# Kernel tuning notes

Measured on AMD Instinct MI355X. Metric: run time of the kernel, lower is better.

The kernel has to match this reference:

```python
import jax, jax.numpy as jnp
import numpy as np

D_MODEL = 768
NUM_HEADS = 12
HEAD_DIM = D_MODEL // NUM_HEADS
B, T = 2, 4096


def setup_inputs() -> dict:
    key = jax.random.key(0)
    k1, k2, k3, k4, k5 = jax.random.split(key, 5)
    s_in = 1.0 / np.sqrt(D_MODEL)
    return {
        "x": jax.random.normal(k1, (B, T, D_MODEL), dtype=jnp.float32),
        "w_qkv": jax.random.normal(k2, (3 * D_MODEL, D_MODEL), dtype=jnp.float32) * s_in,
        "b_qkv": jax.random.normal(k3, (3 * D_MODEL,), dtype=jnp.float32) * 0.01,
        "w_out": jax.random.normal(k4, (D_MODEL, D_MODEL), dtype=jnp.float32) * s_in,
        "b_out": jax.random.normal(k5, (D_MODEL,), dtype=jnp.float32) * 0.01,
    }


def reference(x, w_qkv, b_qkv, w_out, b_out):
    b, t, c = x.shape
    # qkv: [B,T,3C] -> [3,B,H,T,Dh]  (torch Linear: x @ W.T + b)
    qkv = (x @ w_qkv.T + b_qkv).reshape(b, t, 3, NUM_HEADS, HEAD_DIM)
    qkv = jnp.transpose(qkv, (2, 0, 3, 1, 4))
    q, k, v = qkv[0], qkv[1], qkv[2]
    scale = 1.0 / np.sqrt(HEAD_DIM)
    scores = jnp.einsum("bhqd,bhkd->bhqk", q, k) * scale  # [B,H,T,T]
    causal = jnp.tril(jnp.ones((t, t), dtype=bool))
    scores = jnp.where(causal, scores, -jnp.inf)
    weights = jax.nn.softmax(scores, axis=-1)
    out = jnp.einsum("bhqk,bhkd->bhqd", weights, v)  # [B,H,T,Dh]
    out = jnp.transpose(out, (0, 2, 1, 3)).reshape(b, t, c)
    return out @ w_out.T + b_out
```

## Files before the change

kernel.cpp:

```cpp
#include <hip/hip_runtime.h>


#define NHEADS 12
#define DHEAD  64
#define TSEQ   4096
#define BATCH  2
#define CMODEL 768
#define MTOT   (BATCH * TSEQ)
#define NQKV   (3 * CMODEL)

typedef __attribute__((ext_vector_type(8))) short s16x8;
typedef __attribute__((ext_vector_type(4))) float f32x4;
typedef __attribute__((ext_vector_type(4))) unsigned short u16x4;
typedef __attribute__((ext_vector_type(2))) unsigned int u32x2;

__device__ __forceinline__ unsigned short f2bf(float f) {
    unsigned u = __builtin_bit_cast(unsigned, f);
    u += 0x7fffu + ((u >> 16) & 1u);
    return (unsigned short)(u >> 16);
}

__device__ __forceinline__ unsigned pk2bf(float a, float b) {
    return (unsigned)f2bf(a) | ((unsigned)f2bf(b) << 16);
}

__device__ __forceinline__ unsigned pkpos(float a, float b) {
    unsigned ua = __builtin_bit_cast(unsigned, a) + 0x8000u;
    unsigned ub = __builtin_bit_cast(unsigned, b) + 0x8000u;
    return (ua >> 16) | (ub & 0xffff0000u);
}

__device__ __forceinline__ float fexp2(float x) {
    return __builtin_amdgcn_exp2f(x);
}

__device__ __forceinline__ void async_load16(const void* g, void* l) {
    __builtin_amdgcn_global_load_lds(
        (const __attribute__((address_space(1))) unsigned*)g,
        (__attribute__((address_space(3))) unsigned*)l, 16, 0, 0);
}

__global__ __launch_bounds__(256) void cvt3_kernel(
    const float* __restrict__ s0, const float* __restrict__ s1,
    const float* __restrict__ s2,
    unsigned short* __restrict__ d0, unsigned short* __restrict__ d1,
    unsigned short* __restrict__ d2, int n0, int n1, int n2)
{
    int i = blockIdx.x * 256 + threadIdx.x;
    const float* s; unsigned short* d; int j;
    if (i < n0)                { s = s0; d = d0; j = i; }
    else if (i < n0 + n1)      { s = s1; d = d1; j = i - n0; }
    else if (i < n0 + n1 + n2) { s = s2; d = d2; j = i - n0 - n1; }
    else return;
    f32x4 v = ((const f32x4*)s)[j];
    u32x2 o;
    o.x = pk2bf(v.x, v.y);
    o.y = pk2bf(v.z, v.w);
    ((u32x2*)d)[j] = o;
}

__global__ __launch_bounds__(256) void gemm_qkv_kernel(
    const unsigned short* __restrict__ A,
    const unsigned short* __restrict__ Bw,
    const float* __restrict__ bias,
    unsigned short* __restrict__ Qb,
    unsigned short* __restrict__ Kb,
    unsigned short* __restrict__ Vt)
{
    __shared__ unsigned short sA[128][64];
    __shared__ unsigned short sB[128][64];
    const int n0 = blockIdx.x * 128;
    const int m0 = blockIdx.y * 128;
    const int tid = threadIdx.x;
    const int l = tid & 63, g = l >> 4, l15 = l & 15;
    const int w = tid >> 6, wm = w & 1, wn = w >> 1;
    const int wbase = tid & 192;
    const int seg = n0 / 768;

    f32x4 acc[4][4];
#pragma unroll
    for (int a = 0; a < 4; a++)
#pragma unroll
        for (int b = 0; b < 4; b++) acc[a][b] = (f32x4){0.f, 0.f, 0.f, 0.f};

    if (seg < 2) {
        for (int k0 = 0; k0 < 768; k0 += 64) {
#pragma unroll
            for (int i = 0; i < 4; i++) {
                const int idx = i * 256 + tid;
                const int row = idx >> 3, pc = idx & 7;
                const int lc = pc ^ (row & 7);
                async_load16(&A[(size_t)(m0 + row) * 768 + k0 + lc * 8],
                             &sA[0][0] + (size_t)(i * 256 + wbase) * 8);
                async_load16(&Bw[(size_t)(n0 + row) * 768 + k0 + lc * 8],
                             &sB[0][0] + (size_t)(i * 256 + wbase) * 8);
            }
            __syncthreads();
#pragma unroll
            for (int ks = 0; ks < 2; ks++) {
                const int cc = ((ks * 4 + g) ^ (l15 & 7)) * 8;
                s16x8 af[4], bf[4];
#pragma unroll
                for (int mt = 0; mt < 4; mt++)
                    af[mt] = *(const s16x8*)&sA[wm * 64 + mt * 16 + l15][cc];
#pragma unroll
                for (int nt = 0; nt < 4; nt++)
                    bf[nt] = *(const s16x8*)&sB[wn * 64 + nt * 16 + l15][cc];
#pragma unroll
                for (int nt = 0; nt < 4; nt++)
#pragma unroll
                    for (int mt = 0; mt < 4; mt++)
                        acc[nt][mt] = __builtin_amdgcn_mfma_f32_16x16x32_bf16(
                            bf[nt], af[mt], acc[nt][mt], 0, 0, 0);
            }
            __syncthreads();
        }

        unsigned short* dst = (seg == 0) ? Qb : Kb;
        const float sc = (seg == 0) ? 0.18033688011f : 1.0f;
        const int hh = ((n0 - seg * 768) + wn * 64) >> 6;
#pragma unroll
        for (int nt = 0; nt < 4; nt++) {
            const int dh = nt * 16 + g * 4;
            const f32x4 bv4 = *(const f32x4*)&bias[n0 + wn * 64 + dh];
#pragma unroll
            for (int mt = 0; mt < 4; mt++) {
                const int m = m0 + wm * 64 + mt * 16 + l15;
                const int b = m >> 12, t = m & 4095;
                u32x2 pk;
                pk.x = pk2bf((acc[nt][mt][0] + bv4[0]) * sc,
                             (acc[nt][mt][1] + bv4[1]) * sc);
                pk.y = pk2bf((acc[nt][mt][2] + bv4[2]) * sc,
                             (acc[nt][mt][3] + bv4[3]) * sc);
                *(u32x2*)&dst[(((size_t)(b * NHEADS + hh) * TSEQ + t) << 6) + dh] = pk;
            }
        }
    } else {
        for (int k0 = 0; k0 < 768; k0 += 64) {
#pragma unroll
            for (int i = 0; i < 4; i++) {
                const int idx = i * 256 + tid;
                const int row = idx >> 3, pc = idx & 7;
                const int lc = pc ^ (row & 7);
                async_load16(&A[(size_t)(m0 + row) * 768 + k0 + lc * 8],
                             &sA[0][0] + (size_t)(i * 256 + wbase) * 8);
                async_load16(&Bw[(size_t)(n0 + row) * 768 + k0 + lc * 8],
                             &sB[0][0] + (size_t)(i * 256 + wbase) * 8);
            }
            __syncthreads();
#pragma unroll
            for (int ks = 0; ks < 2; ks++) {
                const int cc = ((ks * 4 + g) ^ (l15 & 7)) * 8;
                s16x8 af[4], bf[4];
#pragma unroll
                for (int mt = 0; mt < 4; mt++)
                    af[mt] = *(const s16x8*)&sA[wm * 64 + mt * 16 + l15][cc];
#pragma unroll
                for (int nt = 0; nt < 4; nt++)
                    bf[nt] = *(const s16x8*)&sB[wn * 64 + nt * 16 + l15][cc];
#pragma unroll
                for (int mt = 0; mt < 4; mt++)
#pragma unroll
                    for (int nt = 0; nt < 4; nt++)
                        acc[mt][nt] = __builtin_amdgcn_mfma_f32_16x16x32_bf16(
                            af[mt], bf[nt], acc[mt][nt], 0, 0, 0);
            }
            __syncthreads();
        }

#pragma unroll
        for (int nt = 0; nt < 4; nt++) {
            const int n = n0 + wn * 64 + nt * 16 + l15;
            const float bv = bias[n];
            const int hh = (n - 1536) >> 6;
            const int dh = n & 63;
#pragma unroll
            for (int mt = 0; mt < 4; mt++) {
                const int mg = m0 + wm * 64 + mt * 16 + g * 4;
                const int b = mg >> 12, t = mg & 4095;
                u32x2 pk;
                pk.x = pk2bf(acc[mt][nt][0] + bv, acc[mt][nt][1] + bv);
                pk.y = pk2bf(acc[mt][nt][2] + bv, acc[mt][nt][3] + bv);
                *(u32x2*)&Vt[((size_t)(b * NHEADS + hh) * DHEAD + dh) * TSEQ + t] = pk;
            }
        }
    }
}


__global__ __launch_bounds__(256, 3) void attn_kernel(
    const unsigned short* __restrict__ Qb,
    const unsigned short* __restrict__ Kb,
    const unsigned short* __restrict__ Vt,
    unsigned short* __restrict__ Ob)
{
    __shared__ unsigned short sK[2][64][64];
    __shared__ unsigned short sV[2][64][64];
    __shared__ unsigned short sPT[4][2][16][64];
    const int bh = blockIdx.x;
    const int jq = 31 - blockIdx.y;
    const int q0 = jq * 128;
    const int ntiles = 2 * jq + 2;
    const int tid = threadIdx.x;
    const int w = tid >> 6, l = tid & 63, g = l >> 4, l15 = l & 15;
    const int wbase = tid & 192;
    const int xk = l15 & 7;

    const int qg0 = q0 + w * 32 + l15;
    const int qg1 = qg0 + 16;

    const unsigned short* Qp0 = Qb + ((size_t)bh * TSEQ + qg0) * DHEAD;
    const unsigned short* Qp1 = Qb + ((size_t)bh * TSEQ + qg1) * DHEAD;
    s16x8 qa[2][2];
    qa[0][0] = *(const s16x8*)&Qp0[g * 8];
    qa[0][1] = *(const s16x8*)&Qp0[32 + g * 8];
    qa[1][0] = *(const s16x8*)&Qp1[g * 8];
    qa[1][1] = *(const s16x8*)&Qp1[32 + g * 8];

    s16x8 vones;
#pragma unroll
    for (int e = 0; e < 8; e++) vones[e] = (short)0x3F80;

    f32x4 o[2][4];
#pragma unroll
    for (int nt = 0; nt < 4; nt++) {
        o[0][nt] = (f32x4){0.f, 0.f, 0.f, 0.f};
        o[1][nt] = (f32x4){0.f, 0.f, 0.f, 0.f};
    }
    f32x4 lac[2];
    lac[0] = (f32x4){0.f, 0.f, 0.f, 0.f};
    lac[1] = (f32x4){0.f, 0.f, 0.f, 0.f};

    const unsigned short* Kbase = Kb + (size_t)bh * TSEQ * DHEAD;
    const unsigned short* Vbase = Vt + (size_t)bh * DHEAD * TSEQ;

    auto stage = [&](int jt, int buf) {
        const int kt = jt * 64;
#pragma unroll
        for (int p = 0; p < 2; p++) {
            const int idx = p * 256 + tid;
            const int row = idx >> 3, pc = idx & 7;
            const int lc = pc ^ (row & 7);
            async_load16(&Kbase[(size_t)(kt + row) * DHEAD + lc * 8],
                         &sK[buf][0][0] + (size_t)(p * 256 + wbase) * 8);
            async_load16(&Vbase[(size_t)row * TSEQ + kt + lc * 8],
                         &sV[buf][0][0] + (size_t)(p * 256 + wbase) * 8);
        }
    };

    stage(0, 0);
    __syncthreads();

    for (int jt = 0; jt < ntiles; jt++) {
        const int buf = jt & 1;
        if (jt + 1 < ntiles) stage(jt + 1, buf ^ 1);
        const int kt = jt * 64;

        f32x4 st[2][4];
#pragma unroll
        for (int nt = 0; nt < 4; nt++) {
            st[0][nt] = (f32x4){0.f, 0.f, 0.f, 0.f};
            st[1][nt] = (f32x4){0.f, 0.f, 0.f, 0.f};
        }
#pragma unroll
        for (int ks = 0; ks < 2; ks++) {
            const int cc = ((ks * 4 + g) ^ xk) * 8;
#pragma unroll
            for (int nt = 0; nt < 4; nt++) {
                const s16x8 akf = *(const s16x8*)&sK[buf][nt * 16 + l15][cc];
                st[0][nt] = __builtin_amdgcn_mfma_f32_16x16x32_bf16(
                    akf, qa[0][ks], st[0][nt], 0, 0, 0);
                st[1][nt] = __builtin_amdgcn_mfma_f32_16x16x32_bf16(
                    akf, qa[1][ks], st[1][nt], 0, 0, 0);
            }
        }

        if (jt >= ntiles - 2) {
#pragma unroll
            for (int nt = 0; nt < 4; nt++)
#pragma unroll
                for (int r = 0; r < 4; r++) {
                    const int key = kt + nt * 16 + g * 4 + r;
                    if (key > qg0) st[0][nt][r] = -1e30f;
                    if (key > qg1) st[1][nt][r] = -1e30f;
                }
        }

#pragma unroll
        for (int qf = 0; qf < 2; qf++) {
#pragma unroll
            for (int nt = 0; nt < 4; nt++) {
                float p0 = fexp2(st[qf][nt][0]);
                float p1 = fexp2(st[qf][nt][1]);
                float p2 = fexp2(st[qf][nt][2]);
                float p3 = fexp2(st[qf][nt][3]);
                u32x2 pk;
                pk.x = pkpos(p0, p1);
                pk.y = pkpos(p2, p3);
                const int phys = ((nt * 2 + (g >> 1)) ^ xk) * 8 + (g & 1) * 4;
                *(u32x2*)&sPT[w][qf][l15][phys] = pk;
            }
        }

#pragma unroll
        for (int ks = 0; ks < 2; ks++) {
            const int cc = ((ks * 4 + g) ^ xk) * 8;
            const s16x8 bp0 = *(const s16x8*)&sPT[w][0][l15][cc];
            const s16x8 bp1 = *(const s16x8*)&sPT[w][1][l15][cc];
#pragma unroll
            for (int nt = 0; nt < 4; nt++) {
                const s16x8 avf = *(const s16x8*)&sV[buf][nt * 16 + l15][cc];
                o[0][nt] = __builtin_amdgcn_mfma_f32_16x16x32_bf16(
                    avf, bp0, o[0][nt], 0, 0, 0);
                o[1][nt] = __builtin_amdgcn_mfma_f32_16x16x32_bf16(
                    avf, bp1, o[1][nt], 0, 0, 0);
            }
            lac[0] = __builtin_amdgcn_mfma_f32_16x16x32_bf16(vones, bp0, lac[0], 0, 0, 0);
            lac[1] = __builtin_amdgcn_mfma_f32_16x16x32_bf16(vones, bp1, lac[1], 0, 0, 0);
        }
        __syncthreads();
    }

    const int b = bh / NHEADS, h = bh - b * NHEADS;
#pragma unroll
    for (int qf = 0; qf < 2; qf++) {
        const int qg = (qf == 0) ? qg0 : qg1;
        const float inv = 1.0f / lac[qf][0];
#pragma unroll
        for (int nt = 0; nt < 4; nt++) {
            u32x2 pk;
            pk.x = pk2bf(o[qf][nt][0] * inv, o[qf][nt][1] * inv);
            pk.y = pk2bf(o[qf][nt][2] * inv, o[qf][nt][3] * inv);
            *(u32x2*)&Ob[((size_t)b * TSEQ + qg) * CMODEL + h * DHEAD + nt * 16 + g * 4] = pk;
        }
    }
}

__global__ __launch_bounds__(256) void gemm_out_kernel(
    const unsigned short* __restrict__ A,
    const unsigned short* __restrict__ Bw,
    const float* __restrict__ bias,
    float* __restrict__ out)
{
    __shared__ unsigned short sA[128][64];
    __shared__ unsigned short sB[128][64];
    const int n0 = blockIdx.x * 128;
    const int m0 = blockIdx.y * 128;
    const int tid = threadIdx.x;
    const int l = tid & 63, g = l >> 4, l15 = l & 15;
    const int w = tid >> 6, wm = w & 1, wn = w >> 1;
    const int wbase = tid & 192;

    f32x4 acc[4][4];
#pragma unroll
    for (int mt = 0; mt < 4; mt++)
#pragma unroll
        for (int nt = 0; nt < 4; nt++) acc[mt][nt] = (f32x4){0.f, 0.f, 0.f, 0.f};

    for (int k0 = 0; k0 < 768; k0 += 64) {
#pragma unroll
        for (int i = 0; i < 4; i++) {
            const int idx = i * 256 + tid;
            const int row = idx >> 3, pc = idx & 7;
            const int lc = pc ^ (row & 7);
            async_load16(&A[(size_t)(m0 + row) * 768 + k0 + lc * 8],
                         &sA[0][0] + (size_t)(i * 256 + wbase) * 8);
            async_load16(&Bw[(size_t)(n0 + row) * 768 + k0 + lc * 8],
                         &sB[0][0] + (size_t)(i * 256 + wbase) * 8);
        }
        __syncthreads();
#pragma unroll
        for (int ks = 0; ks < 2; ks++) {
            const int cc = ((ks * 4 + g) ^ (l15 & 7)) * 8;
            s16x8 af[4], bf[4];
#pragma unroll
            for (int mt = 0; mt < 4; mt++)
                af[mt] = *(const s16x8*)&sA[wm * 64 + mt * 16 + l15][cc];
#pragma unroll
            for (int nt = 0; nt < 4; nt++)
                bf[nt] = *(const s16x8*)&sB[wn * 64 + nt * 16 + l15][cc];
#pragma unroll
            for (int mt = 0; mt < 4; mt++)
#pragma unroll
                for (int nt = 0; nt < 4; nt++)
                    acc[mt][nt] = __builtin_amdgcn_mfma_f32_16x16x32_bf16(
                        af[mt], bf[nt], acc[mt][nt], 0, 0, 0);
        }
        __syncthreads();
    }

#pragma unroll
    for (int nt = 0; nt < 4; nt++) {
        const int n = n0 + wn * 64 + nt * 16 + l15;
        const float bv = bias[n];
#pragma unroll
        for (int mt = 0; mt < 4; mt++)
#pragma unroll
            for (int r = 0; r < 4; r++) {
                const int m = m0 + wm * 64 + mt * 16 + g * 4 + r;
                out[(size_t)m * CMODEL + n] = acc[mt][nt][r] + bv;
            }
    }
}

extern "C" void kernel_launch(void* const* d_in, const int* in_sizes, int n_in,
                              void* d_out, int out_size, void* d_ws, size_t ws_size,
                              hipStream_t stream) {
    const float* x     = (const float*)d_in[0];
    const float* w_qkv = (const float*)d_in[1];
    const float* b_qkv = (const float*)d_in[2];
    const float* w_out = (const float*)d_in[3];
    const float* b_out = (const float*)d_in[4];
    float* out = (float*)d_out;

    char* ws = (char*)d_ws;
    size_t off = 0;
    auto alloc = [&](size_t bytes) -> unsigned short* {
        unsigned short* p = (unsigned short*)(ws + off);
        off += (bytes + 255) & ~(size_t)255;
        return p;
    };
    unsigned short* xb    = alloc((size_t)MTOT * CMODEL * 2);
    unsigned short* wqkvb = alloc((size_t)NQKV * CMODEL * 2);
    unsigned short* woutb = alloc((size_t)CMODEL * CMODEL * 2);
    unsigned short* Qb    = alloc((size_t)BATCH * NHEADS * TSEQ * DHEAD * 2);
    unsigned short* Kb    = alloc((size_t)BATCH * NHEADS * TSEQ * DHEAD * 2);
    unsigned short* Vt    = alloc((size_t)BATCH * NHEADS * TSEQ * DHEAD * 2);
    unsigned short* Ob    = alloc((size_t)MTOT * CMODEL * 2);

    const int n40 = MTOT * CMODEL / 4;
    const int n41 = NQKV * CMODEL / 4;
    const int n42 = CMODEL * CMODEL / 4;
    const int nblk = (n40 + n41 + n42 + 255) / 256;
    cvt3_kernel<<<dim3(nblk), 256, 0, stream>>>(
        x, w_qkv, w_out, xb, wqkvb, woutb, n40, n41, n42);

    gemm_qkv_kernel<<<dim3(NQKV / 128, MTOT / 128), 256, 0, stream>>>(
        xb, wqkvb, b_qkv, Qb, Kb, Vt);
    attn_kernel<<<dim3(BATCH * NHEADS, 32), 256, 0, stream>>>(Qb, Kb, Vt, Ob);
    gemm_out_kernel<<<dim3(CMODEL / 128, MTOT / 128), 256, 0, stream>>>(
        Ob, woutb, b_out, out);
}
```

Measured before the change: 239.6 us.

## Balance causal attention work by pairing query blocks and splitting across two workgroups

Each workgroup now processes a short query block together with its mirrored long one, so every workgroup does 33 key tiles instead of 2 to 64. The long block's key range is split between the two workgroups of a pair. Each writes partial fp32 outputs and row sums to a workspace, and the second to finish combines them, coordinated by an atomic counter. That counter is zeroed in the convert kernel. This removes load imbalance and tail effects from the triangular causal workload, at the cost of extra partial-result traffic, fences, atomics and more live registers.

```diff
diff --git a/kernel.cpp b/kernel.cpp
--- a/kernel.cpp
+++ b/kernel.cpp
@@ -8,6 +8,7 @@
 #define CMODEL 768
 #define MTOT   (BATCH * TSEQ)
 #define NQKV   (3 * CMODEL)
+#define NBH    (BATCH * NHEADS)
 
 typedef __attribute__((ext_vector_type(8))) short s16x8;
 typedef __attribute__((ext_vector_type(4))) float f32x4;
@@ -44,9 +45,11 @@
     const float* __restrict__ s0, const float* __restrict__ s1,
     const float* __restrict__ s2,
     unsigned short* __restrict__ d0, unsigned short* __restrict__ d1,
-    unsigned short* __restrict__ d2, int n0, int n1, int n2)
+    unsigned short* __restrict__ d2, int n0, int n1, int n2,
+    unsigned* __restrict__ flags)
 {
     int i = blockIdx.x * 256 + threadIdx.x;
+    if (i < NBH * 16) flags[i] = 0;
     const float* s; unsigned short* d; int j;
     if (i < n0)                { s = s0; d = d0; j = i; }
     else if (i < n0 + n1)      { s = s1; d = d1; j = i - n0; }
@@ -187,151 +190,236 @@
     }
 }
 
+__device__ __forceinline__ void process_tile(
+    const unsigned short (&sKb)[64][64],
+    const unsigned short (&sVb)[64][64],
+    unsigned short (&sPTw)[2][16][64],
+    const s16x8 (&qa)[2][2],
+    f32x4 (&o)[2][4], f32x4 (&lac)[2],
+    s16x8 vones, int kt, int qg0, bool mask, int g, int l15)
+{
+    const int xk = l15 & 7;
+    const int qg1 = qg0 + 16;
+
+    f32x4 st[2][4];
+#pragma unroll
+    for (int nt = 0; nt < 4; nt++) {
+        st[0][nt] = (f32x4){0.f, 0.f, 0.f, 0.f};
+        st[1][nt] = (f32x4){0.f, 0.f, 0.f, 0.f};
+    }
+#pragma unroll
+    for (int ks = 0; ks < 2; ks++) {
+        const int cc = ((ks * 4 + g) ^ xk) * 8;
+#pragma unroll
+        for (int nt = 0; nt < 4; nt++) {
+            const s16x8 akf = *(const s16x8*)&sKb[nt * 16 + l15][cc];
+            st[0][nt] = __builtin_amdgcn_mfma_f32_16x16x32_bf16(
+                akf, qa[0][ks], st[0][nt], 0, 0, 0);
+            st[1][nt] = __builtin_amdgcn_mfma_f32_16x16x32_bf16(
+                akf, qa[1][ks], st[1][nt], 0, 0, 0);
+        }
+    }
+
+    if (mask) {
+#pragma unroll
+        for (int nt = 0; nt < 4; nt++)
+#pragma unroll
+            for (int r = 0; r < 4; r++) {
+                const int key = kt + nt * 16 + g * 4 + r;
+                if (key > qg0) st[0][nt][r] = -1e30f;
+                if (key > qg1) st[1][nt][r] = -1e30f;
+            }
+    }
+
+#pragma unroll
+    for (int qf = 0; qf < 2; qf++) {
+#pragma unroll
+        for (int nt = 0; nt < 4; nt++) {
+            float p0 = fexp2(st[qf][nt][0]);
+            float p1 = fexp2(st[qf][nt][1]);
+            float p2 = fexp2(st[qf][nt][2]);
+            float p3 = fexp2(st[qf][nt][3]);
+            u32x2 pk;
+            pk.x = pkpos(p0, p1);
+            pk.y = pkpos(p2, p3);
+            const int phys = ((nt * 2 + (g >> 1)) ^ xk) * 8 + (g & 1) * 4;
+            *(u32x2*)&sPTw[qf][l15][phys] = pk;
+        }
+    }
+
+#pragma unroll
+    for (int ks = 0; ks < 2; ks++) {
+        const int cc = ((ks * 4 + g) ^ xk) * 8;
+        const s16x8 bp0 = *(const s16x8*)&sPTw[0][l15][cc];
+        const s16x8 bp1 = *(const s16x8*)&sPTw[1][l15][cc];
+#pragma unroll
+        for (int nt = 0; nt < 4; nt++) {
+            const s16x8 avf = *(const s16x8*)&sVb[nt * 16 + l15][cc];
+            o[0][nt] = __builtin_amdgcn_mfma_f32_16x16x32_bf16(
+                avf, bp0, o[0][nt], 0, 0, 0);
+            o[1][nt] = __builtin_amdgcn_mfma_f32_16x16x32_bf16(
+                avf, bp1, o[1][nt], 0, 0, 0);
+        }
+        lac[0] = __builtin_amdgcn_mfma_f32_16x16x32_bf16(vones, bp0, lac[0], 0, 0, 0);
+        lac[1] = __builtin_amdgcn_mfma_f32_16x16x32_bf16(vones, bp1, lac[1], 0, 0, 0);
+    }
+}
 
 __global__ __launch_bounds__(256, 3) void attn_kernel(
     const unsigned short* __restrict__ Qb,
     const unsigned short* __restrict__ Kb,
     const unsigned short* __restrict__ Vt,
-    unsigned short* __restrict__ Ob)
+    unsigned short* __restrict__ Ob,
+    float* __restrict__ oPart,
+    float* __restrict__ lPart,
+    unsigned* __restrict__ flags)
 {
     __shared__ unsigned short sK[2][64][64];
     __shared__ unsigned short sV[2][64][64];
     __shared__ unsigned short sPT[4][2][16][64];
-    const int bh = blockIdx.x;
-    const int jq = 31 - blockIdx.y;
-    const int q0 = jq * 128;
-    const int ntiles = 2 * jq + 2;
+    __shared__ unsigned sOld;
+    const int bh   = blockIdx.x;
+    const int p    = blockIdx.y >> 1;
+    const int half = blockIdx.y & 1;
+    const int jA = p, jB = 31 - p;
+    const int nA = 2 * p + 2;
     const int tid = threadIdx.x;
     const int w = tid >> 6, l = tid & 63, g = l >> 4, l15 = l & 15;
     const int wbase = tid & 192;
-    const int xk = l15 & 7;
-
-    const int qg0 = q0 + w * 32 + l15;
-    const int qg1 = qg0 + 16;
-
-    const unsigned short* Qp0 = Qb + ((size_t)bh * TSEQ + qg0) * DHEAD;
-    const unsigned short* Qp1 = Qb + ((size_t)bh * TSEQ + qg1) * DHEAD;
-    s16x8 qa[2][2];
-    qa[0][0] = *(const s16x8*)&Qp0[g * 8];
-    qa[0][1] = *(const s16x8*)&Qp0[32 + g * 8];
-    qa[1][0] = *(const s16x8*)&Qp1[g * 8];
-    qa[1][1] = *(const s16x8*)&Qp1[32 + g * 8];
+
+    const int rl0  = w * 32 + l15;
+    const int qg0A = jA * 128 + rl0;
+    const int qg0B = jB * 128 + rl0;
+
+    const unsigned short* QpA = Qb + ((size_t)bh * TSEQ + qg0A) * DHEAD;
+    const unsigned short* QpB = Qb + ((size_t)bh * TSEQ + qg0B) * DHEAD;
+    s16x8 qA[2][2], qB[2][2];
+    qA[0][0] = *(const s16x8*)&QpA[g * 8];
+    qA[0][1] = *(const s16x8*)&QpA[32 + g * 8];
+    qA[1][0] = *(const s16x8*)&QpA[16 * DHEAD + g * 8];
+    qA[1][1] = *(const s16x8*)&QpA[16 * DHEAD + 32 + g * 8];
+    qB[0][0] = *(const s16x8*)&QpB[g * 8];
+    qB[0][1] = *(const s16x8*)&QpB[32 + g * 8];
+    qB[1][0] = *(const s16x8*)&QpB[16 * DHEAD + g * 8];
+    qB[1][1] = *(const s16x8*)&QpB[16 * DHEAD + 32 + g * 8];
 
     s16x8 vones;
 #pragma unroll
     for (int e = 0; e < 8; e++) vones[e] = (short)0x3F80;
 
-    f32x4 o[2][4];
+    f32x4 oA[2][4], oB[2][4];
 #pragma unroll
     for (int nt = 0; nt < 4; nt++) {
-        o[0][nt] = (f32x4){0.f, 0.f, 0.f, 0.f};
-        o[1][nt] = (f32x4){0.f, 0.f, 0.f, 0.f};
-    }
-    f32x4 lac[2];
-    lac[0] = (f32x4){0.f, 0.f, 0.f, 0.f};
-    lac[1] = (f32x4){0.f, 0.f, 0.f, 0.f};
+        oA[0][nt] = (f32x4){0.f, 0.f, 0.f, 0.f};
+        oA[1][nt] = (f32x4){0.f, 0.f, 0.f, 0.f};
+        oB[0][nt] = (f32x4){0.f, 0.f, 0.f, 0.f};
+        oB[1][nt] = (f32x4){0.f, 0.f, 0.f, 0.f};
+    }
+    f32x4 lacA[2], lacB[2];
+    lacA[0] = (f32x4){0.f, 0.f, 0.f, 0.f};
+    lacA[1] = (f32x4){0.f, 0.f, 0.f, 0.f};
+    lacB[0] = (f32x4){0.f, 0.f, 0.f, 0.f};
+    lacB[1] = (f32x4){0.f, 0.f, 0.f, 0.f};
 
     const unsigned short* Kbase = Kb + (size_t)bh * TSEQ * DHEAD;
     const unsigned short* Vbase = Vt + (size_t)bh * DHEAD * TSEQ;
 
+    auto tile_of = [&](int s) -> int {
+        if (half == 0) return (s < nA) ? s : (s - nA);
+        return (31 - 2 * p) + s;
+    };
+
     auto stage = [&](int jt, int buf) {
         const int kt = jt * 64;
 #pragma unroll
-        for (int p = 0; p < 2; p++) {
-            const int idx = p * 256 + tid;
+        for (int pp = 0; pp < 2; pp++) {
+            const int idx = pp * 256 + tid;
             const int row = idx >> 3, pc = idx & 7;
             const int lc = pc ^ (row & 7);
             async_load16(&Kbase[(size_t)(kt + row) * DHEAD + lc * 8],
-                         &sK[buf][0][0] + (size_t)(p * 256 + wbase) * 8);
+                         &sK[buf][0][0] + (size_t)(pp * 256 + wbase) * 8);
             async_load16(&Vbase[(size_t)row * TSEQ + kt + lc * 8],
-                         &sV[buf][0][0] + (size_t)(p * 256 + wbase) * 8);
+                         &sV[buf][0][0] + (size_t)(pp * 256 + wbase) * 8);
         }
     };
 
-    stage(0, 0);
+    stage(tile_of(0), 0);
     __syncthreads();
 
-    for (int jt = 0; jt < ntiles; jt++) {
-        const int buf = jt & 1;
-        if (jt + 1 < ntiles) stage(jt + 1, buf ^ 1);
-        const int kt = jt * 64;
-
-        f32x4 st[2][4];
-#pragma unroll
-        for (int nt = 0; nt < 4; nt++) {
-            st[0][nt] = (f32x4){0.f, 0.f, 0.f, 0.f};
-            st[1][nt] = (f32x4){0.f, 0.f, 0.f, 0.f};
-        }
-#pragma unroll
-        for (int ks = 0; ks < 2; ks++) {
-            const int cc = ((ks * 4 + g) ^ xk) * 8;
+    for (int s = 0; s < 33; s++) {
+        const int buf = s & 1;
+        if (s + 1 < 33) stage(tile_of(s + 1), buf ^ 1);
+        const int kt = tile_of(s) * 64;
+
+        const bool selA = (half == 0) && (s < nA);
+        if (selA) {
+            process_tile(sK[buf], sV[buf], sPT[w], qA, oA, lacA, vones,
+                         kt, qg0A, s >= nA - 2, g, l15);
+        } else {
+            const bool mask = (half == 1) && (s >= 31);
+            process_tile(sK[buf], sV[buf], sPT[w], qB, oB, lacB, vones,
+                         kt, qg0B, mask, g, l15);
+        }
+        __syncthreads();
+    }
+
+    const int b = bh / NHEADS, hd = bh - b * NHEADS;
+
+    if (half == 0) {
+#pragma unroll
+        for (int qf = 0; qf < 2; qf++) {
+            const int qg = qg0A + qf * 16;
+            const float inv = 1.0f / lacA[qf][0];
 #pragma unroll
             for (int nt = 0; nt < 4; nt++) {
-                const s16x8 akf = *(const s16x8*)&sK[buf][nt * 16 + l15][cc];
-                st[0][nt] = __builtin_amdgcn_mfma_f32_16x16x32_bf16(
-                    akf, qa[0][ks], st[0][nt], 0, 0, 0);
-                st[1][nt] = __builtin_amdgcn_mfma_f32_16x16x32_bf16(
-                    akf, qa[1][ks], st[1][nt], 0, 0, 0);
-            }
-        }
-
-        if (jt >= ntiles - 2) {
-#pragma unroll
-            for (int nt = 0; nt < 4; nt++)
-#pragma unroll
-                for (int r = 0; r < 4; r++) {
-                    const int key = kt + nt * 16 + g * 4 + r;
-                    if (key > qg0) st[0][nt][r] = -1e30f;
-                    if (key > qg1) st[1][nt][r] = -1e30f;
-                }
-        }
-
+                u32x2 pk;
+                pk.x = pk2bf(oA[qf][nt][0] * inv, oA[qf][nt][1] * inv);
+                pk.y = pk2bf(oA[qf][nt][2] * inv, oA[qf][nt][3] * inv);
+                *(u32x2*)&Ob[((size_t)b * TSEQ + qg) * CMODEL + hd * DHEAD +
+                             nt * 16 + g * 4] = pk;
+            }
+        }
+    }
+
+    const int pairIdx = bh * 16 + p;
+    const size_t slot = (size_t)pairIdx * 2 + half;
+    float* oS = oPart + slot * (128 * 64);
+    float* lS = lPart + slot * 128;
+#pragma unroll
+    for (int qf = 0; qf < 2; qf++) {
+        const int rl = rl0 + qf * 16;
+#pragma unroll
+        for (int nt = 0; nt < 4; nt++)
+            *(f32x4*)&oS[(size_t)rl * 64 + nt * 16 + g * 4] = oB[qf][nt];
+        if (g == 0) lS[rl] = lacB[qf][0];
+    }
+    __syncthreads();
+    if (tid == 0) {
+        __threadfence();
+        sOld = atomicAdd(&flags[pairIdx], 1u);
+    }
+    __syncthreads();
+    if (sOld == 1) {
+        __threadfence();
+        const size_t oslot = (size_t)pairIdx * 2 + (half ^ 1);
+        const float* oO = oPart + oslot * (128 * 64);
+        const float* lO = lPart + oslot * 128;
 #pragma unroll
         for (int qf = 0; qf < 2; qf++) {
+            const int rl = rl0 + qf * 16;
+            const int qg = qg0B + qf * 16;
+            const float inv = 1.0f / (lacB[qf][0] + lO[rl]);
 #pragma unroll
             for (int nt = 0; nt < 4; nt++) {
-                float p0 = fexp2(st[qf][nt][0]);
-                float p1 = fexp2(st[qf][nt][1]);
-                float p2 = fexp2(st[qf][nt][2]);
-                float p3 = fexp2(st[qf][nt][3]);
+                const f32x4 po = *(const f32x4*)&oO[(size_t)rl * 64 + nt * 16 + g * 4];
                 u32x2 pk;
-                pk.x = pkpos(p0, p1);
-                pk.y = pkpos(p2, p3);
-                const int phys = ((nt * 2 + (g >> 1)) ^ xk) * 8 + (g & 1) * 4;
-                *(u32x2*)&sPT[w][qf][l15][phys] = pk;
-            }
-        }
-
-#pragma unroll
-        for (int ks = 0; ks < 2; ks++) {
-            const int cc = ((ks * 4 + g) ^ xk) * 8;
-            const s16x8 bp0 = *(const s16x8*)&sPT[w][0][l15][cc];
-            const s16x8 bp1 = *(const s16x8*)&sPT[w][1][l15][cc];
-#pragma unroll
-            for (int nt = 0; nt < 4; nt++) {
-                const s16x8 avf = *(const s16x8*)&sV[buf][nt * 16 + l15][cc];
-                o[0][nt] = __builtin_amdgcn_mfma_f32_16x16x32_bf16(
-                    avf, bp0, o[0][nt], 0, 0, 0);
-                o[1][nt] = __builtin_amdgcn_mfma_f32_16x16x32_bf16(
-                    avf, bp1, o[1][nt], 0, 0, 0);
-            }
-            lac[0] = __builtin_amdgcn_mfma_f32_16x16x32_bf16(vones, bp0, lac[0], 0, 0, 0);
-            lac[1] = __builtin_amdgcn_mfma_f32_16x16x32_bf16(vones, bp1, lac[1], 0, 0, 0);
-        }
-        __syncthreads();
-    }
-
-    const int b = bh / NHEADS, h = bh - b * NHEADS;
-#pragma unroll
-    for (int qf = 0; qf < 2; qf++) {
-        const int qg = (qf == 0) ? qg0 : qg1;
-        const float inv = 1.0f / lac[qf][0];
-#pragma unroll
-        for (int nt = 0; nt < 4; nt++) {
-            u32x2 pk;
-            pk.x = pk2bf(o[qf][nt][0] * inv, o[qf][nt][1] * inv);
-            pk.y = pk2bf(o[qf][nt][2] * inv, o[qf][nt][3] * inv);
-            *(u32x2*)&Ob[((size_t)b * TSEQ + qg) * CMODEL + h * DHEAD + nt * 16 + g * 4] = pk;
+                pk.x = pk2bf((oB[qf][nt][0] + po[0]) * inv,
+                             (oB[qf][nt][1] + po[1]) * inv);
+                pk.y = pk2bf((oB[qf][nt][2] + po[2]) * inv,
+                             (oB[qf][nt][3] + po[3]) * inv);
+                *(u32x2*)&Ob[((size_t)b * TSEQ + qg) * CMODEL + hd * DHEAD +
+                             nt * 16 + g * 4] = pk;
+            }
         }
     }
 }
@@ -415,29 +503,33 @@
 
     char* ws = (char*)d_ws;
     size_t off = 0;
-    auto alloc = [&](size_t bytes) -> unsigned short* {
-        unsigned short* p = (unsigned short*)(ws + off);
+    auto alloc = [&](size_t bytes) -> void* {
+        void* p = (void*)(ws + off);
         off += (bytes + 255) & ~(size_t)255;
         return p;
     };
-    unsigned short* xb    = alloc((size_t)MTOT * CMODEL * 2);
-    unsigned short* wqkvb = alloc((size_t)NQKV * CMODEL * 2);
-    unsigned short* woutb = alloc((size_t)CMODEL * CMODEL * 2);
-    unsigned short* Qb    = alloc((size_t)BATCH * NHEADS * TSEQ * DHEAD * 2);
-    unsigned short* Kb    = alloc((size_t)BATCH * NHEADS * TSEQ * DHEAD * 2);
-    unsigned short* Vt    = alloc((size_t)BATCH * NHEADS * TSEQ * DHEAD * 2);
-    unsigned short* Ob    = alloc((size_t)MTOT * CMODEL * 2);
+    unsigned short* xb    = (unsigned short*)alloc((size_t)MTOT * CMODEL * 2);
+    unsigned short* wqkvb = (unsigned short*)alloc((size_t)NQKV * CMODEL * 2);
+    unsigned short* woutb = (unsigned short*)alloc((size_t)CMODEL * CMODEL * 2);
+    unsigned short* Qb    = (unsigned short*)alloc((size_t)NBH * TSEQ * DHEAD * 2);
+    unsigned short* Kb    = (unsigned short*)alloc((size_t)NBH * TSEQ * DHEAD * 2);
+    unsigned short* Vt    = (unsigned short*)alloc((size_t)NBH * TSEQ * DHEAD * 2);
+    unsigned short* Ob    = (unsigned short*)alloc((size_t)MTOT * CMODEL * 2);
+    float*    oPart = (float*)alloc((size_t)NBH * 16 * 2 * 128 * 64 * 4);
+    float*    lPart = (float*)alloc((size_t)NBH * 16 * 2 * 128 * 4);
+    unsigned* flags = (unsigned*)alloc((size_t)NBH * 16 * 4);
 
     const int n40 = MTOT * CMODEL / 4;
     const int n41 = NQKV * CMODEL / 4;
     const int n42 = CMODEL * CMODEL / 4;
     const int nblk = (n40 + n41 + n42 + 255) / 256;
     cvt3_kernel<<<dim3(nblk), 256, 0, stream>>>(
-        x, w_qkv, w_out, xb, wqkvb, woutb, n40, n41, n42);
+        x, w_qkv, w_out, xb, wqkvb, woutb, n40, n41, n42, flags);
 
     gemm_qkv_kernel<<<dim3(NQKV / 128, MTOT / 128), 256, 0, stream>>>(
         xb, wqkvb, b_qkv, Qb, Kb, Vt);
-    attn_kernel<<<dim3(BATCH * NHEADS, 32), 256, 0, stream>>>(Qb, Kb, Vt, Ob);
+    attn_kernel<<<dim3(NBH, 32), 256, 0, stream>>>(
+        Qb, Kb, Vt, Ob, oPart, lPart, flags);
     gemm_out_kernel<<<dim3(CMODEL / 128, MTOT / 128), 256, 0, stream>>>(
         Ob, woutb, b_out, out);
 }
```

Result: slower. 424.2 us (+77.1%).
